# Performance work log

Hardware: AMD Instinct MI355X
Metric: run time of the kernel (lower is better)

The kernel has to match this reference:

```python
import jax, jax.numpy as jnp
import numpy as np

B, T, M, P = 512, 64, 256, 256


def setup_inputs() -> dict:
    key = jax.random.key(0)
    ks = jax.random.split(key, 17)
    w = lambda i, shape: (jax.random.normal(ks[i], shape, jnp.float32) * 0.05)
    return {
        "encoded_inputs": jax.random.normal(ks[0], (B, T, M), jnp.float32),
        "y": jax.random.normal(ks[1], (B, T, 1), jnp.float32),
        "tar": jax.random.normal(ks[2], (B, 2), jnp.float32),
        "train": 1,
        "Wd_w": w(3, (M, 2 * P)), "Wd_b": w(4, (M,)),
        "Ud_w": w(5, (M, M)),
        "vd_w": w(6, (1, M)),
        "wt_w": w(7, (1, M + 1)), "wt_b": w(8, (1,)),
        "Wy_w": w(9, (P, P + M)), "Wy_b": w(10, (P,)),
        "vy_w": w(11, (1, P)), "vy_b": w(12, (1,)),
        "Wih": w(13, (4 * P, 1)), "Whh": w(14, (4 * P, P)),
        "bih": w(15, (4 * P,)), "bhh": w(16, (4 * P,)),
    }


def _lstm_cell(x, h, c, Wih, Whh, bih, bhh):
    # torch.nn.LSTMCell gate order: i, f, g, o
    g = x @ Wih.T + h @ Whh.T + (bih + bhh)
    i, f, gg, o = jnp.split(g, 4, axis=1)
    c = jax.nn.sigmoid(f) * c + jax.nn.sigmoid(i) * jnp.tanh(gg)
    h = jax.nn.sigmoid(o) * jnp.tanh(c)
    return h, c


def reference(encoded_inputs, y, tar, train,
              Wd_w, Wd_b, Ud_w, vd_w, wt_w, wt_b,
              Wy_w, Wy_b, vy_w, vy_b, Wih, Whh, bih, bhh):
    Bn = encoded_inputs.shape[0]
    Pn = Whh.shape[1]
    Mn = encoded_inputs.shape[2]
    h0 = jnp.zeros((Bn, Pn), encoded_inputs.dtype)
    c0 = jnp.zeros((Bn, Pn), encoded_inputs.dtype)
    ctx0 = jnp.zeros((Bn, Mn), encoded_inputs.dtype)
    # U_d(encoded_inputs) is loop-invariant
    y1 = jnp.einsum('btm,nm->btn', encoded_inputs, Ud_w)  # (B,T,M)

    def attend(h, s):
        x1 = jnp.concatenate([h, s], axis=1) @ Wd_w.T + Wd_b      # (B,M)
        z1 = jnp.tanh(x1[:, None, :] + y1)                        # (B,T,M)
        l = jnp.einsum('btm,m->bt', z1, vd_w[0])                  # (B,T)
        beta = jax.nn.softmax(l, axis=1)
        return jnp.einsum('bt,btm->bm', beta, encoded_inputs)     # (B,M)

    def step(carry, y_t):
        h, s, _ = carry
        c_t = attend(h, s)
        y_til = jnp.concatenate([c_t, y_t], axis=1) @ wt_w.T + wt_b  # (B,1)
        h, s = _lstm_cell(y_til, h, s, Wih, Whh, bih, bhh)
        return (h, s, c_t), None

    (h, s, c_t), _ = jax.lax.scan(step, (h0, c0, ctx0), jnp.swapaxes(y, 0, 1))

    def head(h):
        return (jnp.concatenate([h, c_t], axis=1) @ Wy_w.T + Wy_b) @ vy_w.T + vy_b

    def extra(h, s, inp):
        y_til = jnp.concatenate([c_t, inp], axis=1) @ wt_w.T + wt_b
        h, s = _lstm_cell(y_til, h, s, Wih, Whh, bih, bhh)
        return h, s, head(h)

    y_Tp1 = head(h)
    if train:
        h, s, y_Tp2 = extra(h, s, tar[:, 0:1])
        h, s, y_Tp3 = extra(h, s, tar[:, 1:2])
    else:
        h, s, y_Tp2 = extra(h, s, y_Tp1)
        h, s, y_Tp3 = extra(h, s, y_Tp2)
    return (y_Tp1, y_Tp2, y_Tp3)
```

## Files before the change

### kernel.cpp

```cpp
#include <hip/hip_runtime.h>


typedef unsigned short u16;
typedef unsigned int u32;
typedef _Float16 half_t;
typedef half_t h2 __attribute__((ext_vector_type(2)));

#define BB 512
#define TT 64
#define MM 256
#define YS 264
#define ES 68
#define NROW 2
#define NTH 1024

#define WD16_OFF  0
#define WHH16_OFF 131072
#define WY16_OFF  393216
#define WQ_ELEMS  524288
#define WQ_BYTES  (WQ_ELEMS * 2)

struct H8 { h2 p[4]; };

#if defined(__has_builtin)
#if __has_builtin(__builtin_amdgcn_fdot2)
#define FDOT2(a, b, c) __builtin_amdgcn_fdot2((a), (b), (c), false)
#endif
#endif
#ifndef FDOT2
__device__ __forceinline__ float FDOT2(h2 a, h2 b, float c) {
  return c + (float)a[0] * (float)b[0] + (float)a[1] * (float)b[1];
}
#endif

__device__ __forceinline__ float dot8(const H8 w, const H8 a, float acc) {
  acc = FDOT2(w.p[0], a.p[0], acc);
  acc = FDOT2(w.p[1], a.p[1], acc);
  acc = FDOT2(w.p[2], a.p[2], acc);
  acc = FDOT2(w.p[3], a.p[3], acc);
  return acc;
}
__device__ __forceinline__ u16 f2h(float f) {
  union { half_t h; u16 u; } x; x.h = (half_t)f; return x.u;
}
__device__ __forceinline__ float h2f(u16 u) {
  union { u16 u; half_t h; } x; x.u = u; return (float)x.h;
}
__device__ __forceinline__ void unpackH8(const H8 v, float f[8]) {
#pragma unroll
  for (int i = 0; i < 8; ++i) f[i] = (float)v.p[i >> 1][i & 1];
}
__device__ __forceinline__ void ldf8(const float* p, float f[8]) {
  float4 a = *(const float4*)p;
  float4 b = *(const float4*)(p + 4);
  f[0]=a.x; f[1]=a.y; f[2]=a.z; f[3]=a.w;
  f[4]=b.x; f[5]=b.y; f[6]=b.z; f[7]=b.w;
}
__device__ __forceinline__ float tanh_fast(float x) {
  float e = __builtin_amdgcn_exp2f(x * 2.885390081777927f);
  return 1.0f - 2.0f * __builtin_amdgcn_rcpf(1.0f + e);
}
__device__ __forceinline__ float sigmoid_fast(float x) {
  float e = __builtin_amdgcn_exp2f(x * -1.4426950408889634f);
  return __builtin_amdgcn_rcpf(1.0f + e);
}

__global__ __launch_bounds__(256) void prep_kernel(
    const float* __restrict__ Wd, const float* __restrict__ Whh,
    const float* __restrict__ Wy, u16* __restrict__ o) {
  int i = blockIdx.x * 256 + threadIdx.x;
  float v;
  if (i < WHH16_OFF) {
    int ki = i & 7, n = (i >> 3) & 255, kb = i >> 11;
    v = Wd[n * 512 + kb * 8 + ki];
  } else if (i < WY16_OFF) {
    int r = i - WHH16_OFF;
    int ki = r & 7, n = (r >> 3) & 1023, kb = r >> 13;
    v = Whh[n * 256 + kb * 8 + ki];
  } else {
    int r = i - WY16_OFF;
    int ki = r & 7, n = (r >> 3) & 255, kb = r >> 11;
    v = Wy[n * 512 + kb * 8 + ki];
  }
  o[i] = f2h(v);
}

template <int WQ>
__global__ __launch_bounds__(NTH, 4) void scan_kernel(
    const float* __restrict__ E,
    const float* __restrict__ yin,
    const float* __restrict__ tar,
    const int*   __restrict__ train,
    const void*  __restrict__ Wd_q,
    const float* __restrict__ Wd_b,
    const float* __restrict__ Ud_w,
    const float* __restrict__ vd_w,
    const float* __restrict__ wt_w,
    const float* __restrict__ wt_b,
    const void*  __restrict__ Wy_q,
    const float* __restrict__ Wy_b,
    const float* __restrict__ vy_w,
    const float* __restrict__ vy_b,
    const float* __restrict__ Wih,
    const void*  __restrict__ Whh_q,
    const float* __restrict__ bih,
    const float* __restrict__ bhh,
    float* __restrict__ out)
{
  __shared__ __align__(16) u16   y1l[NROW][TT * YS];
  __shared__ __align__(16) u16   e16T[NROW][MM * ES];
  __shared__ __align__(16) u32   hs16[NROW][256];
  __shared__ __align__(16) u32   ctx16p[NROW][128];
  __shared__ __align__(16) float px1[8][MM];
  __shared__ __align__(16) u16   pgs[16][MM];
  __shared__ __align__(16) float lpart[NROW][4][TT];
  __shared__ __align__(16) u16   betas16[8][TT];
  __shared__ __align__(16) float ysh[NROW][TT];
  __shared__ float red[16];
  __shared__ float sc[NROW];

  const int j   = threadIdx.x;
  const int n   = j & 255;
  const int grp = j >> 8;
  const int wv  = j >> 6;
  const int b0  = blockIdx.x * NROW;

  if (j < 512) ((u32*)hs16)[j] = 0;
  float creg0 = 0.f, creg1 = 0.f;

  const float wih0 = Wih[n],       wih1 = Wih[n + 256];
  const float wih2 = Wih[n + 512], wih3 = Wih[n + 768];
  const float bb0 = bih[n]       + bhh[n];
  const float bb1 = bih[n + 256] + bhh[n + 256];
  const float bb2 = bih[n + 512] + bhh[n + 512];
  const float bb3 = bih[n + 768] + bhh[n + 768];
  const float wtM = wt_w[MM], wtb = wt_b[0];

  if (j < NROW * TT)
    ysh[j >> 6][j & 63] = yin[(size_t)(b0 + (j >> 6)) * TT + (j & 63)];

  {
    const float* __restrict__ Eb0 = E + (size_t)b0 * TT * MM;
    for (int i = j; i < NROW * TT * MM; i += NTH) {
      int r = i >> 14;
      int idx = i & 16383;
      int t = idx >> 8, m = idx & 255;
      e16T[r][m * ES + t] = f2h(Eb0[i]);
    }
  }

  {
    const int rs = grp >> 1, ths = grp & 1;
    const float* __restrict__ Eb = E + (size_t)(b0 + rs) * TT * MM;
    const float* __restrict__ Uj = Ud_w + (size_t)n * MM;
    for (int t0 = ths * 32; t0 < ths * 32 + 32; t0 += 16) {
      float acc[16];
#pragma unroll
      for (int i = 0; i < 16; ++i) acc[i] = 0.f;
      for (int m0 = 0; m0 < MM; m0 += 8) {
        float w[8]; ldf8(Uj + m0, w);
#pragma unroll
        for (int tt = 0; tt < 16; ++tt) {
          float e[8]; ldf8(Eb + (size_t)(t0 + tt) * MM + m0, e);
#pragma unroll
          for (int mm = 0; mm < 8; ++mm) acc[tt] = fmaf(e[mm], w[mm], acc[tt]);
        }
      }
#pragma unroll
      for (int tt = 0; tt < 16; ++tt)
        y1l[rs][(t0 + tt) * YS + n] = f2h(acc[tt]);
    }
  }
  __syncthreads();

  auto gates_apply = [&](int r, float gi, float gf, float gg, float go,
                         float ytil) {
    gi += ytil * wih0 + bb0;
    gf += ytil * wih1 + bb1;
    gg += ytil * wih2 + bb2;
    go += ytil * wih3 + bb3;
    float& cr = r ? creg1 : creg0;
    float c = sigmoid_fast(gf) * cr + sigmoid_fast(gi) * tanh_fast(gg);
    float h = sigmoid_fast(go) * tanh_fast(c);
    cr = c;
    u16* hsu = (u16*)hs16[r];
    hsu[n] = f2h(h);
    hsu[256 + n] = f2h(c);
  };

  auto whh_gates = [&]() {
    if (wv >= 8) {
      const int jj = j - 512;
      const int n2 = jj & 255, half = jj >> 8;
      float a00 = 0, a01 = 0, a10 = 0, a11 = 0;
      float a20 = 0, a21 = 0, a30 = 0, a31 = 0;
      if (WQ) {
        const u16* __restrict__ base =
            (const u16*)Whh_q + ((size_t)(half * 16) * 1024 + n2) * 8;
#pragma unroll 2
        for (int i = 0; i < 16; ++i) {
          const u16* p = base + (size_t)i * 8192;
          H8 w0 = *(const H8*)p;
          H8 w1 = *(const H8*)(p + 2048);
          H8 w2 = *(const H8*)(p + 4096);
          H8 w3 = *(const H8*)(p + 6144);
          const int kb = half * 16 + i;
          H8 h0v = *(const H8*)&hs16[0][kb * 4];
          H8 h1v = *(const H8*)&hs16[1][kb * 4];
          a00 = dot8(w0, h0v, a00); a01 = dot8(w0, h1v, a01);
          a10 = dot8(w1, h0v, a10); a11 = dot8(w1, h1v, a11);
          a20 = dot8(w2, h0v, a20); a21 = dot8(w2, h1v, a21);
          a30 = dot8(w3, h0v, a30); a31 = dot8(w3, h1v, a31);
        }
      } else {
        const float* __restrict__ base =
            (const float*)Whh_q + (size_t)n2 * 256 + half * 128;
#pragma unroll 2
        for (int i = 0; i < 16; ++i) {
          const int kb = half * 16 + i;
          H8 h0v = *(const H8*)&hs16[0][kb * 4];
          H8 h1v = *(const H8*)&hs16[1][kb * 4];
          float hf0[8], hf1[8]; unpackH8(h0v, hf0); unpackH8(h1v, hf1);
          float w0[8], w1[8], w2[8], w3[8];
          ldf8(base + i * 8, w0);
          ldf8(base + 256 * 256 + i * 8, w1);
          ldf8(base + 512 * 256 + i * 8, w2);
          ldf8(base + 768 * 256 + i * 8, w3);
#pragma unroll
          for (int m = 0; m < 8; ++m) {
            a00 = fmaf(hf0[m], w0[m], a00); a01 = fmaf(hf1[m], w0[m], a01);
            a10 = fmaf(hf0[m], w1[m], a10); a11 = fmaf(hf1[m], w1[m], a11);
            a20 = fmaf(hf0[m], w2[m], a20); a21 = fmaf(hf1[m], w2[m], a21);
            a30 = fmaf(hf0[m], w3[m], a30); a31 = fmaf(hf1[m], w3[m], a31);
          }
        }
      }
      const int hb = half << 1;
      pgs[(0 << 2) | hb | 0][n2] = f2h(a00);
      pgs[(0 << 2) | hb | 1][n2] = f2h(a01);
      pgs[(1 << 2) | hb | 0][n2] = f2h(a10);
      pgs[(1 << 2) | hb | 1][n2] = f2h(a11);
      pgs[(2 << 2) | hb | 0][n2] = f2h(a20);
      pgs[(2 << 2) | hb | 1][n2] = f2h(a21);
      pgs[(3 << 2) | hb | 0][n2] = f2h(a30);
      pgs[(3 << 2) | hb | 1][n2] = f2h(a31);
    }
  };

  auto gates_combine_apply = [&](float yt0, float yt1) {
    float gi0 = h2f(pgs[0][n]) + h2f(pgs[2][n]);
    float gf0 = h2f(pgs[4][n]) + h2f(pgs[6][n]);
    float gg0 = h2f(pgs[8][n]) + h2f(pgs[10][n]);
    float go0 = h2f(pgs[12][n]) + h2f(pgs[14][n]);
    gates_apply(0, gi0, gf0, gg0, go0, yt0);
    float gi1 = h2f(pgs[1][n]) + h2f(pgs[3][n]);
    float gf1 = h2f(pgs[5][n]) + h2f(pgs[7][n]);
    float gg1 = h2f(pgs[9][n]) + h2f(pgs[11][n]);
    float go1 = h2f(pgs[13][n]) + h2f(pgs[15][n]);
    gates_apply(1, gi1, gf1, gg1, go1, yt1);
  };

  auto head_store = [&](int outIdx) {
    float p = 0.f;
    const int rr = grp >> 1, seg = grp & 1;
    const u32* st = seg ? ctx16p[rr] : hs16[rr];
    if (WQ) {
      const u16* pw = (const u16*)Wy_q + ((size_t)(seg * 32) * 256 + n) * 8;
#pragma unroll 2
      for (int kb = 0; kb < 32; ++kb) {
        H8 w = *(const H8*)pw; pw += 2048;
        H8 s = *(const H8*)&st[kb * 4];
        p = dot8(w, s, p);
      }
    } else {
      const float* W = (const float*)Wy_q + (size_t)n * 512 + seg * 256;
#pragma unroll 2
      for (int kb = 0; kb < 32; ++kb) {
        H8 sv = *(const H8*)&st[kb * 4];
        float sf[8]; unpackH8(sv, sf);
        float w[8]; ldf8(W + kb * 8, w);
#pragma unroll
        for (int i = 0; i < 8; ++i) p = fmaf(sf[i], w[i], p);
      }
    }
    if (grp) px1[grp - 1][n] = p;
    __syncthreads();
    if (grp == 0) {
      float q0 = (p + px1[0][n] + Wy_b[n]) * vy_w[n];
      float q1 = (px1[1][n] + px1[2][n] + Wy_b[n]) * vy_w[n];
#pragma unroll
      for (int off = 32; off; off >>= 1) {
        q0 += __shfl_xor(q0, off, 64);
        q1 += __shfl_xor(q1, off, 64);
      }
      if ((j & 63) == 0) { red[wv] = q0; red[4 + wv] = q1; }
    }
    __syncthreads();
    if (j == 0) {
      float o0 = red[0] + red[1] + red[2] + red[3] + vy_b[0];
      float o1 = red[4] + red[5] + red[6] + red[7] + vy_b[0];
      out[(size_t)outIdx * BB + b0] = o0;
      out[(size_t)outIdx * BB + b0 + 1] = o1;
      sc[0] = o0; sc[1] = o1;
    }
    __syncthreads();
  };

  for (int step = 0; step < TT; ++step) {
    {
      float ax0 = 0.f, ax1 = 0.f;
      if (WQ) {
        const u16* pd = (const u16*)Wd_q + ((size_t)(grp * 16) * 256 + n) * 8;
#pragma unroll 4
        for (int i = 0; i < 16; ++i) {
          H8 w = *(const H8*)pd; pd += 2048;
          const int kb = grp * 16 + i;
          H8 s0 = *(const H8*)&hs16[0][kb * 4];
          H8 s1 = *(const H8*)&hs16[1][kb * 4];
          ax0 = dot8(w, s0, ax0);
          ax1 = dot8(w, s1, ax1);
        }
      } else {
        const float* pd = (const float*)Wd_q + (size_t)n * 512 + grp * 128;
#pragma unroll 2
        for (int i = 0; i < 16; ++i) {
          const int kb = grp * 16 + i;
          H8 s0v = *(const H8*)&hs16[0][kb * 4];
          H8 s1v = *(const H8*)&hs16[1][kb * 4];
          float f0[8], f1[8]; unpackH8(s0v, f0); unpackH8(s1v, f1);
          float w[8]; ldf8(pd + i * 8, w);
#pragma unroll
          for (int m = 0; m < 8; ++m) {
            ax0 = fmaf(f0[m], w[m], ax0);
            ax1 = fmaf(f1[m], w[m], ax1);
          }
        }
      }
      if (grp == 0) { float b = Wd_b[n]; ax0 += b; ax1 += b; }
      px1[grp][n] = ax0;
      px1[4 + grp][n] = ax1;
    }
    __syncthreads();

    if (wv < 8) {
      const int r = j >> 8, e4 = (j >> 6) & 3, t = j & 63;
      const int mb = e4 * 64;
      const u16* __restrict__ yrow = &y1l[r][t * YS + mb];
      const float* __restrict__ p0 = &px1[(r << 2) | 0][mb];
      const float* __restrict__ p1 = &px1[(r << 2) | 1][mb];
      const float* __restrict__ p2 = &px1[(r << 2) | 2][mb];
      const float* __restrict__ p3 = &px1[(r << 2) | 3][mb];
      const float* __restrict__ vp = vd_w + mb;
      float lp = 0.f;
#pragma unroll 2
      for (int m0 = 0; m0 < 64; m0 += 8) {
        float xa[8], xb[8], xc[8], xd[8], vf[8], yf[8];
        ldf8(p0 + m0, xa); ldf8(p1 + m0, xb);
        ldf8(p2 + m0, xc); ldf8(p3 + m0, xd);
        H8 yv = *(const H8*)(yrow + m0); unpackH8(yv, yf);
        ldf8(vp + m0, vf);
#pragma unroll
        for (int mm = 0; mm < 8; ++mm) {
          float z = tanh_fast(xa[mm] + xb[mm] + xc[mm] + xd[mm] + yf[mm]);
          lp = fmaf(z, vf[mm], lp);
        }
      }
      lpart[r][e4][t] = lp;
    } else {
      whh_gates();
    }
    __syncthreads();

    if (j < 512) {
      const int r = j >> 8, lane = j & 63;
      float l = lpart[r][0][lane] + lpart[r][1][lane] + lpart[r][2][lane] +
                lpart[r][3][lane];
      float mx = l;
#pragma unroll
      for (int off = 32; off; off >>= 1) mx = fmaxf(mx, __shfl_xor(mx, off, 64));
      float e = __builtin_amdgcn_exp2f((l - mx) * 1.4426950408889634f);
      float sm = e;
#pragma unroll
      for (int off = 32; off; off >>= 1) sm += __shfl_xor(sm, off, 64);
      betas16[wv][lane] = f2h(e * __builtin_amdgcn_rcpf(sm));
      asm volatile("s_waitcnt lgkmcnt(0)" ::: "memory");
      const u16* __restrict__ bp = betas16[wv];
      const u16* __restrict__ ep = &e16T[r][n * ES];
      float acc = 0.f;
#pragma unroll
      for (int t0 = 0; t0 < TT; t0 += 8) {
        H8 bv = *(const H8*)(bp + t0);
        h2 e0 = *(const h2*)(ep + t0);
        h2 e1 = *(const h2*)(ep + t0 + 2);
        h2 e2 = *(const h2*)(ep + t0 + 4);
        h2 e3 = *(const h2*)(ep + t0 + 6);
        acc = FDOT2(bv.p[0], e0, acc);
        acc = FDOT2(bv.p[1], e1, acc);
        acc = FDOT2(bv.p[2], e2, acc);
        acc = FDOT2(bv.p[3], e3, acc);
      }
      ((u16*)ctx16p[r])[n] = f2h(acc);
      float p = acc * wt_w[n];
#pragma unroll
      for (int off = 32; off; off >>= 1) p += __shfl_xor(p, off, 64);
      if ((j & 63) == 0) red[wv] = p;
    }
    __syncthreads();

    if (j < 256) {
      float yt0 = red[0] + red[1] + red[2] + red[3] + ysh[0][step] * wtM + wtb;
      float yt1 = red[4] + red[5] + red[6] + red[7] + ysh[1][step] * wtM + wtb;
      gates_combine_apply(yt0, yt1);
    }
    __syncthreads();
  }

  if (j < 512) {
    const int r = j >> 8;
    float p = h2f(((const u16*)ctx16p[r])[n]) * wt_w[n];
#pragma unroll
    for (int off = 32; off; off >>= 1) p += __shfl_xor(p, off, 64);
    if ((j & 63) == 0) red[wv] = p;
  }
  __syncthreads();
  const float ctd0 = red[0] + red[1] + red[2] + red[3];
  const float ctd1 = red[4] + red[5] + red[6] + red[7];

  head_store(0);

  const int tr = train[0];
  for (int e = 0; e < 2; ++e) {
    whh_gates();
    __syncthreads();
    if (j < 256) {
      float inp0 = tr ? tar[(size_t)b0 * 2 + e] : sc[0];
      float inp1 = tr ? tar[(size_t)(b0 + 1) * 2 + e] : sc[1];
      float yt0 = ctd0 + inp0 * wtM + wtb;
      float yt1 = ctd1 + inp1 * wtM + wtb;
      gates_combine_apply(yt0, yt1);
    }
    __syncthreads();
    head_store(1 + e);
  }
}

extern "C" void kernel_launch(void* const* d_in, const int* in_sizes, int n_in,
                              void* d_out, int out_size, void* d_ws, size_t ws_size,
                              hipStream_t stream) {
  const float* E     = (const float*)d_in[0];
  const float* yin   = (const float*)d_in[1];
  const float* tar   = (const float*)d_in[2];
  const int*   train = (const int*)d_in[3];
  const float* Wd_w  = (const float*)d_in[4];
  const float* Wd_b  = (const float*)d_in[5];
  const float* Ud_w  = (const float*)d_in[6];
  const float* vd_w  = (const float*)d_in[7];
  const float* wt_w  = (const float*)d_in[8];
  const float* wt_b  = (const float*)d_in[9];
  const float* Wy_w  = (const float*)d_in[10];
  const float* Wy_b  = (const float*)d_in[11];
  const float* vy_w  = (const float*)d_in[12];
  const float* vy_b  = (const float*)d_in[13];
  const float* Wih   = (const float*)d_in[14];
  const float* Whh   = (const float*)d_in[15];
  const float* bih   = (const float*)d_in[16];
  const float* bhh   = (const float*)d_in[17];

  float* out = (float*)d_out;

  if (ws_size >= (size_t)WQ_BYTES) {
    u16* wq = (u16*)d_ws;
    prep_kernel<<<dim3(WQ_ELEMS / 256), dim3(256), 0, stream>>>(
        Wd_w, Whh, Wy_w, wq);
    scan_kernel<1><<<dim3(BB / NROW), dim3(NTH), 0, stream>>>(
        E, yin, tar, train, wq + WD16_OFF, Wd_b, Ud_w, vd_w, wt_w, wt_b,
        wq + WY16_OFF, Wy_b, vy_w, vy_b, Wih, wq + WHH16_OFF, bih, bhh, out);
  } else {
    scan_kernel<0><<<dim3(BB / NROW), dim3(NTH), 0, stream>>>(
        E, yin, tar, train, Wd_w, Wd_b, Ud_w, vd_w, wt_w, wt_b,
        Wy_w, Wy_b, vy_w, vy_b, Wih, Whh, bih, bhh, out);
  }

  (void)in_sizes; (void)n_in; (void)out_size;
}
```

Baseline: 1.078 ms.

## Precompute E·wt per timestep so per-step context vector is skipped in the recurrence

The LSTM input y_til only needs wt·ctx, which equals the softmax-weighted sum of precomputed E[t]·wt. Each step now computes that scalar with wavefront shuffles, removing the per-step 256-wide context dot over T and one block barrier. The full context vector is computed once after the loop for the head. The gate partials are also packed two rows per 32-bit LDS word. This uses fp32 E·wt instead of the fp16 context path, which changes rounding slightly.

```diff
diff --git a/kernel.cpp b/kernel.cpp
--- a/kernel.cpp
+++ b/kernel.cpp
@@ -45,6 +45,14 @@
 }
 __device__ __forceinline__ float h2f(u16 u) {
   union { u16 u; half_t h; } x; x.u = u; return (float)x.h;
+}
+__device__ __forceinline__ u32 pack2h(float a, float b) {
+  union { h2 h; u32 u; } x;
+  x.h[0] = (half_t)a; x.h[1] = (half_t)b;
+  return x.u;
+}
+__device__ __forceinline__ h2 u2h2(u32 u) {
+  union { u32 u; h2 h; } x; x.u = u; return x.h;
 }
 __device__ __forceinline__ void unpackH8(const H8 v, float f[8]) {
 #pragma unroll
@@ -112,10 +120,11 @@
   __shared__ __align__(16) u32   hs16[NROW][256];
   __shared__ __align__(16) u32   ctx16p[NROW][128];
   __shared__ __align__(16) float px1[8][MM];
-  __shared__ __align__(16) u16   pgs[16][MM];
+  __shared__ __align__(16) u32   pgs32[8][MM];
   __shared__ __align__(16) float lpart[NROW][4][TT];
   __shared__ __align__(16) u16   betas16[8][TT];
   __shared__ __align__(16) float ysh[NROW][TT];
+  __shared__ __align__(16) float ewl[NROW][TT];
   __shared__ float red[16];
   __shared__ float sc[NROW];
 
@@ -136,8 +145,19 @@
   const float bb3 = bih[n + 768] + bhh[n + 768];
   const float wtM = wt_w[MM], wtb = wt_b[0];
 
-  if (j < NROW * TT)
-    ysh[j >> 6][j & 63] = yin[(size_t)(b0 + (j >> 6)) * TT + (j & 63)];
+  if (j < NROW * TT) {
+    const int r = j >> 6, t = j & 63;
+    ysh[r][t] = yin[(size_t)(b0 + r) * TT + t];
+    const float* __restrict__ Er = E + ((size_t)(b0 + r) * TT + t) * MM;
+    float acc = 0.f;
+    for (int m0 = 0; m0 < MM; m0 += 8) {
+      float e[8], w[8];
+      ldf8(Er + m0, e); ldf8(wt_w + m0, w);
+#pragma unroll
+      for (int m = 0; m < 8; ++m) acc = fmaf(e[m], w[m], acc);
+    }
+    ewl[r][t] = acc;
+  }
 
   {
     const float* __restrict__ Eb0 = E + (size_t)b0 * TT * MM;
@@ -235,29 +255,22 @@
           }
         }
       }
-      const int hb = half << 1;
-      pgs[(0 << 2) | hb | 0][n2] = f2h(a00);
-      pgs[(0 << 2) | hb | 1][n2] = f2h(a01);
-      pgs[(1 << 2) | hb | 0][n2] = f2h(a10);
-      pgs[(1 << 2) | hb | 1][n2] = f2h(a11);
-      pgs[(2 << 2) | hb | 0][n2] = f2h(a20);
-      pgs[(2 << 2) | hb | 1][n2] = f2h(a21);
-      pgs[(3 << 2) | hb | 0][n2] = f2h(a30);
-      pgs[(3 << 2) | hb | 1][n2] = f2h(a31);
+      pgs32[(0 << 1) | half][n2] = pack2h(a00, a01);
+      pgs32[(1 << 1) | half][n2] = pack2h(a10, a11);
+      pgs32[(2 << 1) | half][n2] = pack2h(a20, a21);
+      pgs32[(3 << 1) | half][n2] = pack2h(a30, a31);
     }
   };
 
   auto gates_combine_apply = [&](float yt0, float yt1) {
-    float gi0 = h2f(pgs[0][n]) + h2f(pgs[2][n]);
-    float gf0 = h2f(pgs[4][n]) + h2f(pgs[6][n]);
-    float gg0 = h2f(pgs[8][n]) + h2f(pgs[10][n]);
-    float go0 = h2f(pgs[12][n]) + h2f(pgs[14][n]);
-    gates_apply(0, gi0, gf0, gg0, go0, yt0);
-    float gi1 = h2f(pgs[1][n]) + h2f(pgs[3][n]);
-    float gf1 = h2f(pgs[5][n]) + h2f(pgs[7][n]);
-    float gg1 = h2f(pgs[9][n]) + h2f(pgs[11][n]);
-    float go1 = h2f(pgs[13][n]) + h2f(pgs[15][n]);
-    gates_apply(1, gi1, gf1, gg1, go1, yt1);
+    h2 i0 = u2h2(pgs32[0][n]), i1 = u2h2(pgs32[1][n]);
+    h2 f0 = u2h2(pgs32[2][n]), f1 = u2h2(pgs32[3][n]);
+    h2 g0 = u2h2(pgs32[4][n]), g1 = u2h2(pgs32[5][n]);
+    h2 o0 = u2h2(pgs32[6][n]), o1 = u2h2(pgs32[7][n]);
+    gates_apply(0, (float)i0[0] + (float)i1[0], (float)f0[0] + (float)f1[0],
+                (float)g0[0] + (float)g1[0], (float)o0[0] + (float)o1[0], yt0);
+    gates_apply(1, (float)i0[1] + (float)i1[1], (float)f0[1] + (float)f1[1],
+                (float)g0[1] + (float)g1[1], (float)o0[1] + (float)o1[1], yt1);
   };
 
   auto head_store = [&](int outIdx) {
@@ -371,49 +384,65 @@
     }
     __syncthreads();
 
-    if (j < 512) {
-      const int r = j >> 8, lane = j & 63;
-      float l = lpart[r][0][lane] + lpart[r][1][lane] + lpart[r][2][lane] +
-                lpart[r][3][lane];
-      float mx = l;
-#pragma unroll
-      for (int off = 32; off; off >>= 1) mx = fmaxf(mx, __shfl_xor(mx, off, 64));
-      float e = __builtin_amdgcn_exp2f((l - mx) * 1.4426950408889634f);
-      float sm = e;
-#pragma unroll
-      for (int off = 32; off; off >>= 1) sm += __shfl_xor(sm, off, 64);
-      betas16[wv][lane] = f2h(e * __builtin_amdgcn_rcpf(sm));
-      asm volatile("s_waitcnt lgkmcnt(0)" ::: "memory");
-      const u16* __restrict__ bp = betas16[wv];
-      const u16* __restrict__ ep = &e16T[r][n * ES];
-      float acc = 0.f;
-#pragma unroll
-      for (int t0 = 0; t0 < TT; t0 += 8) {
-        H8 bv = *(const H8*)(bp + t0);
-        h2 e0 = *(const h2*)(ep + t0);
-        h2 e1 = *(const h2*)(ep + t0 + 2);
-        h2 e2 = *(const h2*)(ep + t0 + 4);
-        h2 e3 = *(const h2*)(ep + t0 + 6);
-        acc = FDOT2(bv.p[0], e0, acc);
-        acc = FDOT2(bv.p[1], e1, acc);
-        acc = FDOT2(bv.p[2], e2, acc);
-        acc = FDOT2(bv.p[3], e3, acc);
-      }
-      ((u16*)ctx16p[r])[n] = f2h(acc);
-      float p = acc * wt_w[n];
-#pragma unroll
-      for (int off = 32; off; off >>= 1) p += __shfl_xor(p, off, 64);
-      if ((j & 63) == 0) red[wv] = p;
-    }
-    __syncthreads();
-
     if (j < 256) {
-      float yt0 = red[0] + red[1] + red[2] + red[3] + ysh[0][step] * wtM + wtb;
-      float yt1 = red[4] + red[5] + red[6] + red[7] + ysh[1][step] * wtM + wtb;
+      const int t = j & 63;
+      float l0 = lpart[0][0][t] + lpart[0][1][t] + lpart[0][2][t] +
+                 lpart[0][3][t];
+      float l1 = lpart[1][0][t] + lpart[1][1][t] + lpart[1][2][t] +
+                 lpart[1][3][t];
+      float m0v = l0, m1v = l1;
+#pragma unroll
+      for (int off = 32; off; off >>= 1) {
+        m0v = fmaxf(m0v, __shfl_xor(m0v, off, 64));
+        m1v = fmaxf(m1v, __shfl_xor(m1v, off, 64));
+      }
+      float e0 = __builtin_amdgcn_exp2f((l0 - m0v) * 1.4426950408889634f);
+      float e1 = __builtin_amdgcn_exp2f((l1 - m1v) * 1.4426950408889634f);
+      float se0 = e0, sy0 = e0 * ewl[0][t];
+      float se1 = e1, sy1 = e1 * ewl[1][t];
+#pragma unroll
+      for (int off = 32; off; off >>= 1) {
+        se0 += __shfl_xor(se0, off, 64); sy0 += __shfl_xor(sy0, off, 64);
+        se1 += __shfl_xor(se1, off, 64); sy1 += __shfl_xor(sy1, off, 64);
+      }
+      float yt0 = sy0 * __builtin_amdgcn_rcpf(se0) + ysh[0][step] * wtM + wtb;
+      float yt1 = sy1 * __builtin_amdgcn_rcpf(se1) + ysh[1][step] * wtM + wtb;
       gates_combine_apply(yt0, yt1);
     }
     __syncthreads();
   }
+
+  if (j < 512) {
+    const int r = j >> 8, lane = j & 63;
+    float l = lpart[r][0][lane] + lpart[r][1][lane] + lpart[r][2][lane] +
+              lpart[r][3][lane];
+    float mx = l;
+#pragma unroll
+    for (int off = 32; off; off >>= 1) mx = fmaxf(mx, __shfl_xor(mx, off, 64));
+    float e = __builtin_amdgcn_exp2f((l - mx) * 1.4426950408889634f);
+    float sm = e;
+#pragma unroll
+    for (int off = 32; off; off >>= 1) sm += __shfl_xor(sm, off, 64);
+    betas16[wv][lane] = f2h(e * __builtin_amdgcn_rcpf(sm));
+    asm volatile("s_waitcnt lgkmcnt(0)" ::: "memory");
+    const u16* __restrict__ bp = betas16[wv];
+    const u16* __restrict__ ep = &e16T[r][n * ES];
+    float acc = 0.f;
+#pragma unroll
+    for (int t0 = 0; t0 < TT; t0 += 8) {
+      H8 bv = *(const H8*)(bp + t0);
+      h2 e0 = *(const h2*)(ep + t0);
+      h2 e1 = *(const h2*)(ep + t0 + 2);
+      h2 e2 = *(const h2*)(ep + t0 + 4);
+      h2 e3 = *(const h2*)(ep + t0 + 6);
+      acc = FDOT2(bv.p[0], e0, acc);
+      acc = FDOT2(bv.p[1], e1, acc);
+      acc = FDOT2(bv.p[2], e2, acc);
+      acc = FDOT2(bv.p[3], e3, acc);
+    }
+    ((u16*)ctx16p[r])[n] = f2h(acc);
+  }
+  __syncthreads();
 
   if (j < 512) {
     const int r = j >> 8;
```

New measurement: 1.046 ms. -2.9%, faster.
